# Kernel optimization log

Measured on AMD Instinct MI355X. Metric: run time of the kernel, lower is better.

The kernel has to match this reference:

```python
import jax, jax.numpy as jnp
import numpy as np

H, N, S, R, CH, LMAX = 512, 32, 1, 1, 1, 1024


def _to_c(x):
    # torch.view_as_real storage -> complex
    return x[..., 0] + 1j * x[..., 1]


def _rep(x, v):
    # einops: '... t n -> ... (v t) n'  (tile trainable copies up to H)
    shp = x.shape
    x = jnp.broadcast_to(x[..., None, :, :], shp[:-2] + (v,) + shp[-2:])
    return x.reshape(shp[:-2] + (v * shp[-2], shp[-1]))


def setup_inputs() -> dict:
    key = jax.random.key(0)
    k1, k2, k3, k4, k5 = jax.random.split(key, 5)
    # dt log-uniform in [1e-3, 1e-1] (S4 default init)
    log_dt = jax.random.uniform(k1, (H,), jnp.float32,
                                minval=float(np.log(1e-3)), maxval=float(np.log(1e-1)))
    # real_type='exp': w_real = -exp(inv_w_real); init around -0.5
    inv_w_real = jnp.log(0.5) * jnp.ones((S, N), jnp.float32) \
        + 0.1 * jax.random.normal(k2, (S, N), jnp.float32)
    w_imag = jnp.broadcast_to(jnp.pi * jnp.arange(N, dtype=jnp.float32), (S, N))
    B_ri = jax.random.normal(k3, (1, S, N, 2), jnp.float32)
    C_ri = jax.random.normal(k4, (CH, H, N, 2), jnp.float32)
    P_ri = 0.5 * jax.random.normal(k5, (R, S, N, 2), jnp.float32)
    return {"log_dt": log_dt, "inv_w_real": inv_w_real, "w_imag": w_imag,
            "B_ri": B_ri, "C_ri": C_ri, "P_ri": P_ri, "L": LMAX}


def _kernel(log_dt, inv_w_real, w_imag, B_ri, C_ri, P_ri, L):
    dt = jnp.exp(log_dt)                                    # (H,)
    w = -jnp.exp(inv_w_real) + 1j * w_imag                  # (S, N), real_type='exp'
    B = _to_c(B_ri)                                         # (1, S, N)
    C = _to_c(C_ri)                                         # (c, H, N)
    P = _to_c(P_ri)                                         # (R, S, N)
    Q = jnp.conj(P)
    v_rep = log_dt.shape[0] // w.shape[0]                   # broadcast = H // S
    B, P, Q = _rep(B, v_rep), _rep(P, v_rep), _rep(Q, v_rep)
    w = _rep(w, v_rep)                                      # (H, N)
    rank = P.shape[0]

    # FFT nodes and bilinear-transformed nodes
    Lf = L // 2 + 1
    omega = jnp.exp(-2j * jnp.pi * jnp.arange(Lf) / L).astype(jnp.complex64)
    z = 2 * (1 - omega) / (1 + omega)                       # (Lf,)

    # Stack B with P and C with Q for batched Cauchy
    Bst = jnp.concatenate([B, P], axis=-3)                  # (1+R, H, N)
    Cst = jnp.concatenate([C, Q], axis=-3)                  # (c+R, H, N)
    v = Bst[:, None] * Cst[None]                            # (1+R, c+R, H, N)
    w_dt = w * dt[:, None]                                  # (H, N): dt folded into A

    # Cauchy kernel with conjugate-pair extension: sum_n v/(z-w) + conj(v)/(z-conj(w))
    v2 = jnp.concatenate([v, jnp.conj(v)], axis=-1)         # (1+R, c+R, H, 2N)
    w2 = jnp.concatenate([w_dt, jnp.conj(w_dt)], axis=-1)   # (H, 2N)
    r = jnp.sum(v2[..., None] / (z - w2[..., :, None]), axis=-2)  # (1+R, c+R, H, Lf)
    r = r * dt[None, None, :, None]

    # Woodbury correction for the low-rank part
    r00 = r[:-rank, :-rank]                                 # (1, c, H, Lf)
    r01 = r[:-rank, -rank:]                                 # (1, R, H, Lf)
    r10 = r[-rank:, :-rank]                                 # (R, c, H, Lf)
    r11 = r[-rank:, -rank:]                                 # (R, R, H, Lf)
    r11 = jnp.moveaxis(r11, (0, 1), (-2, -1))               # (H, Lf, R, R)
    r11 = jnp.linalg.inv(jnp.eye(rank, dtype=r.dtype) + r11)
    r11 = jnp.moveaxis(r11, (-2, -1), (0, 1))               # (R, R, H, Lf)
    k_f = r00 - jnp.einsum('ijhl,jkhl,kmhl->imhl', r01, r11, r10)

    # Undo bilinear transform and go to time domain
    k_f = k_f * 2 / (1 + omega)
    k = jnp.fft.irfft(k_f, n=L, axis=-1)[..., :L]           # (1, c, H, L) real
    return k[-1]                                            # k_B: (c, H, L)


def reference(log_dt, inv_w_real, w_imag, B_ri, C_ri, P_ri, L):
    return _kernel(log_dt, inv_w_real, w_imag, B_ri, C_ri, P_ri, L)
```

## Files before the change

kernel.cpp:

```cpp
#include <hip/hip_runtime.h>
#include <math.h>

#define H_DIM 512
#define N_DIM 32
#define L_LEN 1024

typedef float v2f __attribute__((ext_vector_type(2)));
__device__ __forceinline__ v2f splat2(float a) { return (v2f){a, a}; }


__launch_bounds__(576, 7)
__global__ void ssk_nplr_kernel(const float* __restrict__ log_dt,
                                const float* __restrict__ inv_w_real,
                                const float* __restrict__ w_imag,
                                const float* __restrict__ B_ri,
                                const float* __restrict__ C_ri,
                                const float* __restrict__ P_ri,
                                float* __restrict__ out)
{
    __shared__ float2 Ksh[513];
    __shared__ float2 polD[N_DIM];
    __shared__ float4 polA[N_DIM];
    __shared__ float4 polB[N_DIM];
    __shared__ float  Sre[512], Sim[512];
    __shared__ float  Tre[512], Tim[512];

    const int t = threadIdx.x;
    const int h = blockIdx.x;
    const float dt = expf(log_dt[h]);

    if (t < N_DIM) {
        const int n = t;
        float wr = -expf(inv_w_real[n]);
        float wi = w_imag[n];
        float wdx = wr * dt, wdy = wi * dt;
        float Bx = B_ri[2*n],               By = B_ri[2*n+1];
        float Cx = C_ri[h*2*N_DIM + 2*n],   Cy = C_ri[h*2*N_DIM + 2*n+1];
        float Px = P_ri[2*n],               Py = P_ri[2*n+1];
        float v00x = Bx*Cx - By*Cy, v00y = Bx*Cy + By*Cx;
        float v01x = Bx*Px + By*Py, v01y = By*Px - Bx*Py;
        float v10x = Px*Cx - Py*Cy, v10y = Px*Cy + Py*Cx;
        float v11x = Px*Px + Py*Py;
        polD[n] = make_float2(-2.0f*wdx, wdx*wdx + wdy*wdy);
        polA[n] = make_float4(2.0f*v00x, 2.0f*v01x, 2.0f*v10x, 2.0f*v11x);
        polB[n] = make_float4(2.0f*(v00x*wdx + v00y*wdy),
                              2.0f*(v01x*wdx + v01y*wdy),
                              2.0f*(v10x*wdx + v10y*wdy),
                              2.0f*(v11x*wdx));
    }
    __syncthreads();

    const int j = (t < 512) ? t : 512;
    float si, co;
    if (j == 512) {
        si = 8.7422777e-8f;
        co = -1.0f;
    } else {
        float rev = (float)j * (-0.0009765625f);
        si = __builtin_amdgcn_sinf(rev);
        co = __builtin_amdgcn_cosf(rev);
    }

    float px = 1.0f + co, py = si;
    float pinv = 1.0f / (px*px + py*py);
    float ipx = px*pinv, ipy = -py*pinv;
    float mx = 1.0f - co, my = -si;
    float zx = 2.0f*(mx*ipx - my*ipy);
    float zy = 2.0f*(mx*ipy + my*ipx);

    v2f Z  = { zx, zy };
    v2f Z2 = { zx*zx - zy*zy, 2.0f*zx*zy };

    v2f U0{0,0}, U1{0,0}, U2{0,0}, U3{0,0};
    v2f V0{0,0}, V1{0,0}, V2{0,0}, V3{0,0};
    #pragma unroll 4
    for (int n = 0; n < N_DIM; ++n) {
        float2 d  = polD[n];
        float4 A  = polA[n];
        float4 Bv = polB[n];
        v2f D = __builtin_elementwise_fma(splat2(d.x), Z, Z2);
        D.x += d.y;
        float s  = __builtin_amdgcn_rcpf(fmaf(D.x, D.x, D.y*D.y));
        v2f R = { D.x * s, -(D.y * s) };
        U0 = __builtin_elementwise_fma(splat2(A.x),  R, U0);
        U1 = __builtin_elementwise_fma(splat2(A.y),  R, U1);
        U2 = __builtin_elementwise_fma(splat2(A.z),  R, U2);
        U3 = __builtin_elementwise_fma(splat2(A.w),  R, U3);
        V0 = __builtin_elementwise_fma(splat2(Bv.x), R, V0);
        V1 = __builtin_elementwise_fma(splat2(Bv.y), R, V1);
        V2 = __builtin_elementwise_fma(splat2(Bv.z), R, V2);
        V3 = __builtin_elementwise_fma(splat2(Bv.w), R, V3);
    }
    float r00x = dt*(zx*U0.x - zy*U0.y - V0.x), r00y = dt*(zx*U0.y + zy*U0.x - V0.y);
    float r01x = dt*(zx*U1.x - zy*U1.y - V1.x), r01y = dt*(zx*U1.y + zy*U1.x - V1.y);
    float r10x = dt*(zx*U2.x - zy*U2.y - V2.x), r10y = dt*(zx*U2.y + zy*U2.x - V2.y);
    float r11x = dt*(zx*U3.x - zy*U3.y - V3.x), r11y = dt*(zx*U3.y + zy*U3.x - V3.y);

    float dnx = 1.0f + r11x, dny = r11y;
    float dinv = 1.0f / (dnx*dnx + dny*dny);
    float idx_ = dnx*dinv, idy = -dny*dinv;
    float m01x = r01x*r10x - r01y*r10y;
    float m01y = r01x*r10y + r01y*r10x;
    float kfx = r00x - (m01x*idx_ - m01y*idy);
    float kfy = r00y - (m01x*idy + m01y*idx_);
    float fxv = 2.0f*(kfx*ipx - kfy*ipy);
    float fyv = 2.0f*(kfx*ipy + kfy*ipx);
    if (t <= 512) Ksh[j] = make_float2(fxv, fyv);
    __syncthreads();

    float xr = 0.0f, xi = 0.0f;
    if (t < 512) {
        float2 Ka = Ksh[t];
        float2 Kb = Ksh[512 - t];
        const int tb = t ^ 256;
        float2 Kc = Ksh[tb];
        float2 Kd = Ksh[512 - tb];
        float Wx = co, Wy = -si;
        float hsx = 0.5f*(Ka.x + Kb.x), hsy = 0.5f*(Ka.y - Kb.y);
        float hdx = 0.5f*(Ka.x - Kb.x), hdy = 0.5f*(Ka.y + Kb.y);
        float Yax = hsx - Wy*hdx - Wx*hdy;
        float Yay = hsy - Wy*hdy + Wx*hdx;
        float Wbx = (t < 256) ? -Wy :  Wy;
        float Wby = (t < 256) ?  Wx : -Wx;
        float hsx2 = 0.5f*(Kc.x + Kd.x), hsy2 = 0.5f*(Kc.y - Kd.y);
        float hdx2 = 0.5f*(Kc.x - Kd.x), hdy2 = 0.5f*(Kc.y + Kd.y);
        float Ybx = hsx2 - Wby*hdx2 - Wbx*hdy2;
        float Yby = hsy2 - Wby*hdy2 + Wbx*hdx2;
        if (t & 256) {
            float dr = Ybx - Yax, di = Yby - Yay;
            float wrev = (float)(t & 255) * (1.0f/512.0f);
            float ws = __builtin_amdgcn_sinf(wrev);
            float wc = __builtin_amdgcn_cosf(wrev);
            xr = dr*wc - di*ws; xi = dr*ws + di*wc;
        } else {
            xr = Yax + Ybx; xi = Yay + Yby;
        }
        Sre[t] = xr; Sim[t] = xi;
    }
    __syncthreads();

    if (t < 512) {
        float pr = Sre[t ^ 128], pi_ = Sim[t ^ 128];
        if (t & 128) {
            float dr = pr - xr, di = pi_ - xi;
            float wrev = (float)(t & 127) * (1.0f/256.0f);
            float ws = __builtin_amdgcn_sinf(wrev);
            float wc = __builtin_amdgcn_cosf(wrev);
            xr = dr*wc - di*ws; xi = dr*ws + di*wc;
        } else { xr += pr; xi += pi_; }
        Tre[t] = xr; Tim[t] = xi;
    }
    __syncthreads();

    if (t < 512) {
        float pr = Tre[t ^ 64], pi_ = Tim[t ^ 64];
        if (t & 64) {
            float dr = pr - xr, di = pi_ - xi;
            float wrev = (float)(t & 63) * (1.0f/128.0f);
            float ws = __builtin_amdgcn_sinf(wrev);
            float wc = __builtin_amdgcn_cosf(wrev);
            xr = dr*wc - di*ws; xi = dr*ws + di*wc;
        } else { xr += pr; xi += pi_; }

        #define FFT_STAGE(S_) {                                             \
            float pr2 = __shfl_xor(xr, S_), pi2 = __shfl_xor(xi, S_);       \
            if (t & S_) {                                                   \
                float dr = pr2 - xr, di = pi2 - xi;                         \
                float wrev = (float)(t & (S_-1)) * (0.5f/(float)S_);        \
                float ws = __builtin_amdgcn_sinf(wrev);                     \
                float wc = __builtin_amdgcn_cosf(wrev);                     \
                xr = dr*wc - di*ws; xi = dr*ws + di*wc;                     \
            } else { xr += pr2; xi += pi2; }                                \
        }
        FFT_STAGE(32)
        FFT_STAGE(16)
        FFT_STAGE(8)
        FFT_STAGE(4)
        FFT_STAGE(2)
        #undef FFT_STAGE
        {
            float pr2 = __shfl_xor(xr, 1), pi2 = __shfl_xor(xi, 1);
            if (t & 1) { xr = pr2 - xr; xi = pi2 - xi; }
            else       { xr += pr2; xi += pi2; }
        }
        unsigned m = __brev((unsigned)t) >> 23;
        ((float2*)out)[h*512 + m] = make_float2(xr*(1.0f/512.0f), xi*(1.0f/512.0f));
    }
}

extern "C" void kernel_launch(void* const* d_in, const int* in_sizes, int n_in,
                              void* d_out, int out_size, void* d_ws, size_t ws_size,
                              hipStream_t stream) {
    const float* log_dt     = (const float*)d_in[0];
    const float* inv_w_real = (const float*)d_in[1];
    const float* w_imag     = (const float*)d_in[2];
    const float* B_ri       = (const float*)d_in[3];
    const float* C_ri       = (const float*)d_in[4];
    const float* P_ri       = (const float*)d_in[5];

    ssk_nplr_kernel<<<H_DIM, 576, 0, stream>>>(log_dt, inv_w_real, w_imag,
                                               B_ri, C_ri, P_ri, (float*)d_out);
}
```

Baseline: 15.63 us.

## Restructure inverse FFT into radix-4 stages with precomputed twiddles

The radix-2 butterfly stages of the 512-point inverse FFT are fused pairwise into radix-4 style steps. Each thread now computes its partner values directly from shared memory or lane shuffles, which drops one shared-memory stage, its barrier and the Tre/Tim buffers. All per-stage twiddle sin/cos values are computed up front, before the first barrier, so they overlap the setup phase. In exchange there are more shuffles and shared loads per stage, more live registers, and a lower occupancy hint in launch_bounds.

```diff
diff --git a/kernel.cpp b/kernel.cpp
--- a/kernel.cpp
+++ b/kernel.cpp
@@ -9,7 +9,7 @@
 __device__ __forceinline__ v2f splat2(float a) { return (v2f){a, a}; }
 
 
-__launch_bounds__(576, 7)
+__launch_bounds__(576, 5)
 __global__ void ssk_nplr_kernel(const float* __restrict__ log_dt,
                                 const float* __restrict__ inv_w_real,
                                 const float* __restrict__ w_imag,
@@ -23,7 +23,6 @@
     __shared__ float4 polA[N_DIM];
     __shared__ float4 polB[N_DIM];
     __shared__ float  Sre[512], Sim[512];
-    __shared__ float  Tre[512], Tim[512];
 
     const int t = threadIdx.x;
     const int h = blockIdx.x;
@@ -48,7 +47,25 @@
                               2.0f*(v10x*wdx + v10y*wdy),
                               2.0f*(v11x*wdx));
     }
-    __syncthreads();
+
+    float w256c, w256s, w128c, w128s, w64c, w64s;
+    float w32c, w32s, w16c, w16s, w8c, w8s, w4c, w4s;
+    {
+        float r256 = (float)(t & 255) * (1.0f/512.0f);
+        float r128 = (float)(t & 127) * (1.0f/256.0f);
+        float r64  = (float)(t &  63) * (1.0f/128.0f);
+        float r32  = (float)(t &  31) * (1.0f/64.0f);
+        float r16  = (float)(t &  15) * (1.0f/32.0f);
+        float r8   = (float)(t &   7) * (1.0f/16.0f);
+        float r4   = (float)(t &   3) * (1.0f/8.0f);
+        w256s = __builtin_amdgcn_sinf(r256); w256c = __builtin_amdgcn_cosf(r256);
+        w128s = __builtin_amdgcn_sinf(r128); w128c = __builtin_amdgcn_cosf(r128);
+        w64s  = __builtin_amdgcn_sinf(r64);  w64c  = __builtin_amdgcn_cosf(r64);
+        w32s  = __builtin_amdgcn_sinf(r32);  w32c  = __builtin_amdgcn_cosf(r32);
+        w16s  = __builtin_amdgcn_sinf(r16);  w16c  = __builtin_amdgcn_cosf(r16);
+        w8s   = __builtin_amdgcn_sinf(r8);   w8c   = __builtin_amdgcn_cosf(r8);
+        w4s   = __builtin_amdgcn_sinf(r4);   w4c   = __builtin_amdgcn_cosf(r4);
+    }
 
     const int j = (t < 512) ? t : 512;
     float si, co;
@@ -60,6 +77,7 @@
         si = __builtin_amdgcn_sinf(rev);
         co = __builtin_amdgcn_cosf(rev);
     }
+    __syncthreads();
 
     float px = 1.0f + co, py = si;
     float pinv = 1.0f / (px*px + py*py);
@@ -128,10 +146,7 @@
         float Yby = hsy2 - Wby*hdy2 + Wbx*hdx2;
         if (t & 256) {
             float dr = Ybx - Yax, di = Yby - Yay;
-            float wrev = (float)(t & 255) * (1.0f/512.0f);
-            float ws = __builtin_amdgcn_sinf(wrev);
-            float wc = __builtin_amdgcn_cosf(wrev);
-            xr = dr*wc - di*ws; xi = dr*ws + di*wc;
+            xr = dr*w256c - di*w256s; xi = dr*w256s + di*w256c;
         } else {
             xr = Yax + Ybx; xi = Yay + Yby;
         }
@@ -140,49 +155,73 @@
     __syncthreads();
 
     if (t < 512) {
-        float pr = Sre[t ^ 128], pi_ = Sim[t ^ 128];
-        if (t & 128) {
-            float dr = pr - xr, di = pi_ - xi;
-            float wrev = (float)(t & 127) * (1.0f/256.0f);
-            float ws = __builtin_amdgcn_sinf(wrev);
-            float wc = __builtin_amdgcn_cosf(wrev);
-            xr = dr*wc - di*ws; xi = dr*ws + di*wc;
-        } else { xr += pr; xi += pi_; }
-        Tre[t] = xr; Tim[t] = xi;
-    }
-    __syncthreads();
-
-    if (t < 512) {
-        float pr = Tre[t ^ 64], pi_ = Tim[t ^ 64];
-        if (t & 64) {
-            float dr = pr - xr, di = pi_ - xi;
-            float wrev = (float)(t & 63) * (1.0f/128.0f);
-            float ws = __builtin_amdgcn_sinf(wrev);
-            float wc = __builtin_amdgcn_cosf(wrev);
-            xr = dr*wc - di*ws; xi = dr*ws + di*wc;
-        } else { xr += pr; xi += pi_; }
-
-        #define FFT_STAGE(S_) {                                             \
-            float pr2 = __shfl_xor(xr, S_), pi2 = __shfl_xor(xi, S_);       \
-            if (t & S_) {                                                   \
-                float dr = pr2 - xr, di = pi2 - xi;                         \
-                float wrev = (float)(t & (S_-1)) * (0.5f/(float)S_);        \
-                float ws = __builtin_amdgcn_sinf(wrev);                     \
-                float wc = __builtin_amdgcn_cosf(wrev);                     \
-                xr = dr*wc - di*ws; xi = dr*ws + di*wc;                     \
-            } else { xr += pr2; xi += pi2; }                                \
-        }
-        FFT_STAGE(32)
-        FFT_STAGE(16)
-        FFT_STAGE(8)
-        FFT_STAGE(4)
-        FFT_STAGE(2)
-        #undef FFT_STAGE
         {
-            float pr2 = __shfl_xor(xr, 1), pi2 = __shfl_xor(xi, 1);
-            if (t & 1) { xr = pr2 - xr; xi = pi2 - xi; }
-            else       { xr += pr2; xi += pi2; }
-        }
+            float p1r = Sre[t ^ 128], p1i = Sim[t ^ 128];
+            float p2r = Sre[t ^  64], p2i = Sim[t ^  64];
+            float p3r = Sre[t ^ 192], p3i = Sim[t ^ 192];
+            float Atr, Ati, Apr, Api;
+            if (t & 128) {
+                float dr = p1r - xr, di = p1i - xi;
+                Atr = dr*w128c - di*w128s; Ati = dr*w128s + di*w128c;
+                float er = p3r - p2r, ei = p3i - p2i;
+                float wpr = (t & 64) ?  w128s : -w128s;
+                float wpi = (t & 64) ? -w128c :  w128c;
+                Apr = er*wpr - ei*wpi; Api = er*wpi + ei*wpr;
+            } else {
+                Atr = xr + p1r;  Ati = xi + p1i;
+                Apr = p2r + p3r; Api = p2i + p3i;
+            }
+            if (t & 64) {
+                float dr = Apr - Atr, di = Api - Ati;
+                xr = dr*w64c - di*w64s; xi = dr*w64s + di*w64c;
+            } else { xr = Atr + Apr; xi = Ati + Api; }
+        }
+
+        #define RADIX4S(S_, W1C, W1S, W2C, W2S) {                               \
+            float p1r = __shfl_xor(xr, S_),        p1i = __shfl_xor(xi, S_);    \
+            float p2r = __shfl_xor(xr, S_/2),      p2i = __shfl_xor(xi, S_/2);  \
+            float p3r = __shfl_xor(xr, S_ + S_/2), p3i = __shfl_xor(xi, S_ + S_/2); \
+            float Atr, Ati, Apr, Api;                                           \
+            if (t & S_) {                                                       \
+                float dr = p1r - xr, di = p1i - xi;                             \
+                Atr = dr*W1C - di*W1S; Ati = dr*W1S + di*W1C;                   \
+                float er = p3r - p2r, ei = p3i - p2i;                           \
+                float wpr = (t & (S_/2)) ?  W1S : -W1S;                         \
+                float wpi = (t & (S_/2)) ? -W1C :  W1C;                         \
+                Apr = er*wpr - ei*wpi; Api = er*wpi + ei*wpr;                   \
+            } else {                                                            \
+                Atr = xr + p1r;  Ati = xi + p1i;                                \
+                Apr = p2r + p3r; Api = p2i + p3i;                               \
+            }                                                                   \
+            if (t & (S_/2)) {                                                   \
+                float dr = Apr - Atr, di = Api - Ati;                           \
+                xr = dr*W2C - di*W2S; xi = dr*W2S + di*W2C;                     \
+            } else { xr = Atr + Apr; xi = Ati + Api; }                          \
+        }
+        RADIX4S(32, w32c, w32s, w16c, w16s)
+        RADIX4S(8,  w8c,  w8s,  w4c,  w4s)
+        #undef RADIX4S
+
+        {
+            float p1r = __shfl_xor(xr, 2), p1i = __shfl_xor(xi, 2);
+            float p2r = __shfl_xor(xr, 1), p2i = __shfl_xor(xi, 1);
+            float p3r = __shfl_xor(xr, 3), p3i = __shfl_xor(xi, 3);
+            float Atr, Ati, Apr, Api;
+            if (t & 2) {
+                float dr = p1r - xr, di = p1i - xi;
+                float er = p3r - p2r, ei = p3i - p2i;
+                if (t & 1) { Atr = -di; Ati =  dr;
+                             Apr =  er; Api =  ei; }
+                else       { Atr =  dr; Ati =  di;
+                             Apr = -ei; Api =  er; }
+            } else {
+                Atr = xr + p1r;  Ati = xi + p1i;
+                Apr = p2r + p3r; Api = p2i + p3i;
+            }
+            if (t & 1) { xr = Apr - Atr; xi = Api - Ati; }
+            else       { xr = Atr + Apr; xi = Ati + Api; }
+        }
+
         unsigned m = __brev((unsigned)t) >> 23;
         ((float2*)out)[h*512 + m] = make_float2(xr*(1.0f/512.0f), xi*(1.0f/512.0f));
     }
```

New measurement: 15.86 us. About the same (+1.5%).
